# Kernel optimization log

Measured on AMD Instinct MI355X. Metric: run time of the kernel, lower is better.

The kernel has to match this reference:

```python
import jax, jax.numpy as jnp
import numpy as np

T, N, DIM, DSTATE = 64, 10000, 128, 16

def setup_inputs() -> dict:
    key = jax.random.key(0)
    ks = jax.random.split(key, 5)
    sequence = jax.random.normal(ks[0], (T, N, DIM), dtype=jnp.float32)
    # Diagonal SISO SSM parameters per channel: A is a stable decay in (0,1)
    A = jax.random.uniform(ks[1], (DIM, DSTATE), dtype=jnp.float32, minval=0.1, maxval=0.99)
    B = jax.random.normal(ks[2], (DIM, DSTATE), dtype=jnp.float32) * 0.1
    C = jax.random.normal(ks[3], (DIM, DSTATE), dtype=jnp.float32) * 0.1
    D = jax.random.normal(ks[4], (DIM,), dtype=jnp.float32) * 0.1
    return {"sequence": sequence, "A": A, "B": B, "C": C, "D": D}

def reference(sequence, A, B, C, D):
    # sequence: [T, N, dim]; A,B,C: [dim, d_state]; D: [dim]
    # Per-timestep diagonal SISO cell:
    #   h_t = A * h_{t-1} + B * x_t        (h: [N, dim, d_state])
    #   y_t = sum_s(C * h_t) + D * x_t     (y: [N, dim])
    n = sequence.shape[1]
    h0 = jnp.zeros((n, A.shape[0], A.shape[1]), dtype=sequence.dtype)

    def step(h, x):
        h = A[None] * h + B[None] * x[..., None]
        y = jnp.einsum('nds,ds->nd', h, C) + D[None] * x
        return h, y

    _, outputs = jax.lax.scan(step, h0, sequence)
    return outputs  # [T, N, dim]
```

## Files before the change

kernel.cpp:

```cpp
#include <hip/hip_runtime.h>


constexpr int T_STEPS = 64;
constexpr int DIM = 128;
constexpr int DSTATE = 16;
constexpr int CH = 8;
constexpr int S_FIX = 10000 * 128;

template <int S>
__global__ __launch_bounds__(256) void graph_ssm_kernel(
    const float* __restrict__ seq,
    const float* __restrict__ A,
    const float* __restrict__ B,
    const float* __restrict__ C,
    const float* __restrict__ Dp,
    float* __restrict__ out)
{
    const int tid = blockIdx.x * blockDim.x + threadIdx.x;
    if (tid >= S) return;
    const int d = tid & (DIM - 1);

    float a[DSTATE], cb[DSTATE], g[DSTATE];
#pragma unroll
    for (int s = 0; s < DSTATE; ++s) {
        a[s]  = A[d * DSTATE + s];
        cb[s] = C[d * DSTATE + s] * B[d * DSTATE + s];
        g[s]  = 0.0f;
    }
    float dd = Dp[d];

#pragma unroll
    for (int s = 0; s < DSTATE; ++s) {
        asm volatile("" : "+v"(a[s]), "+v"(cb[s]));
    }
    asm volatile("" : "+v"(dd));

    const float* sp = seq + tid;
    float* op = out + tid;

    auto step = [&](int t, float x) {
        float y0 = dd * x, y1 = 0.f;
#pragma unroll
        for (int s = 0; s < DSTATE; s += 2) {
            g[s + 0] = fmaf(a[s + 0], g[s + 0], x);
            y0 = fmaf(cb[s + 0], g[s + 0], y0);
            g[s + 1] = fmaf(a[s + 1], g[s + 1], x);
            y1 = fmaf(cb[s + 1], g[s + 1], y1);
        }
        __builtin_nontemporal_store(y0 + y1, op + (size_t)t * S);
    };

    float xb[CH], xn[CH];
#pragma unroll
    for (int j = 0; j < CH; ++j) xb[j] = sp[(size_t)j * S];

#pragma unroll 1
    for (int tc = 0; tc < T_STEPS - CH; tc += CH) {
#pragma unroll
        for (int j = 0; j < CH; ++j) xn[j] = sp[(size_t)(tc + CH + j) * S];
#pragma unroll
        for (int j = 0; j < CH; ++j) step(tc + j, xb[j]);
#pragma unroll
        for (int j = 0; j < CH; ++j) xb[j] = xn[j];
    }
#pragma unroll
    for (int j = 0; j < CH; ++j) step(T_STEPS - CH + j, xb[j]);
}

__global__ __launch_bounds__(256) void graph_ssm_kernel_dyn(
    const float* __restrict__ seq, const float* __restrict__ A,
    const float* __restrict__ B, const float* __restrict__ C,
    const float* __restrict__ Dp, float* __restrict__ out, int S)
{
    const int tid = blockIdx.x * blockDim.x + threadIdx.x;
    if (tid >= S) return;
    const int d = tid & (DIM - 1);
    float a[DSTATE], cb[DSTATE], g[DSTATE];
#pragma unroll
    for (int s = 0; s < DSTATE; ++s) {
        a[s]  = A[d * DSTATE + s];
        cb[s] = C[d * DSTATE + s] * B[d * DSTATE + s];
        g[s]  = 0.0f;
    }
    float dd = Dp[d];
#pragma unroll
    for (int s = 0; s < DSTATE; ++s) asm volatile("" : "+v"(a[s]), "+v"(cb[s]));
    asm volatile("" : "+v"(dd));
    const float* sp = seq + tid;
    float* op = out + tid;
    float x = sp[0];
    for (int t = 0; t < T_STEPS; ++t) {
        float xnext = (t + 1 < T_STEPS) ? sp[(size_t)(t + 1) * S] : 0.f;
        float y0 = dd * x, y1 = 0.f;
#pragma unroll
        for (int s = 0; s < DSTATE; s += 2) {
            g[s + 0] = fmaf(a[s + 0], g[s + 0], x);
            y0 = fmaf(cb[s + 0], g[s + 0], y0);
            g[s + 1] = fmaf(a[s + 1], g[s + 1], x);
            y1 = fmaf(cb[s + 1], g[s + 1], y1);
        }
        __builtin_nontemporal_store(y0 + y1, op + (size_t)t * S);
        x = xnext;
    }
}

extern "C" void kernel_launch(void* const* d_in, const int* in_sizes, int n_in,
                              void* d_out, int out_size, void* d_ws, size_t ws_size,
                              hipStream_t stream) {
    const float* seq = (const float*)d_in[0];
    const float* A   = (const float*)d_in[1];
    const float* B   = (const float*)d_in[2];
    const float* C   = (const float*)d_in[3];
    const float* Dp  = (const float*)d_in[4];
    float* out = (float*)d_out;

    const int S = in_sizes[0] / T_STEPS;
    const int block = 256;
    const int grid = (S + block - 1) / block;
    if (S == S_FIX) {
        graph_ssm_kernel<S_FIX><<<grid, block, 0, stream>>>(seq, A, B, C, Dp, out);
    } else {
        graph_ssm_kernel_dyn<<<grid, block, 0, stream>>>(seq, A, B, C, Dp, out, S);
    }
}
```

Baseline: 554.1 us.

## Process two channels per thread with float2 loads and ping-pong buffering

Each thread now handles two adjacent channels, so reads and writes become float2 vector accesses and the grid is halved. The prefetch is restructured into two alternating CH=4 buffers, and nontemporal stores are replaced with ordinary stores. The goal is fewer, wider memory instructions and more independent FMA chains per thread, at the cost of roughly twice the register state and fewer resident threads.

```diff
diff --git a/kernel.cpp b/kernel.cpp
--- a/kernel.cpp
+++ b/kernel.cpp
@@ -4,11 +4,11 @@
 constexpr int T_STEPS = 64;
 constexpr int DIM = 128;
 constexpr int DSTATE = 16;
-constexpr int CH = 8;
+constexpr int CH = 4;
 constexpr int S_FIX = 10000 * 128;
 
 template <int S>
-__global__ __launch_bounds__(256) void graph_ssm_kernel(
+__global__ __launch_bounds__(256) void graph_ssm_kernel2(
     const float* __restrict__ seq,
     const float* __restrict__ A,
     const float* __restrict__ B,
@@ -16,55 +16,71 @@
     const float* __restrict__ Dp,
     float* __restrict__ out)
 {
+    constexpr int S2 = S / 2;
     const int tid = blockIdx.x * blockDim.x + threadIdx.x;
-    if (tid >= S) return;
-    const int d = tid & (DIM - 1);
+    if (tid >= S2) return;
+    const int d0 = (tid * 2) & (DIM - 1);
 
-    float a[DSTATE], cb[DSTATE], g[DSTATE];
+    float a[2][DSTATE], cb[2][DSTATE], g[2][DSTATE];
 #pragma unroll
-    for (int s = 0; s < DSTATE; ++s) {
-        a[s]  = A[d * DSTATE + s];
-        cb[s] = C[d * DSTATE + s] * B[d * DSTATE + s];
-        g[s]  = 0.0f;
+    for (int c = 0; c < 2; ++c) {
+#pragma unroll
+        for (int s = 0; s < DSTATE; ++s) {
+            a[c][s]  = A[(d0 + c) * DSTATE + s];
+            cb[c][s] = C[(d0 + c) * DSTATE + s] * B[(d0 + c) * DSTATE + s];
+            g[c][s]  = 0.0f;
+        }
     }
-    float dd = Dp[d];
+    float dd0 = Dp[d0], dd1 = Dp[d0 + 1];
 
 #pragma unroll
-    for (int s = 0; s < DSTATE; ++s) {
-        asm volatile("" : "+v"(a[s]), "+v"(cb[s]));
-    }
-    asm volatile("" : "+v"(dd));
+    for (int c = 0; c < 2; ++c)
+#pragma unroll
+        for (int s = 0; s < DSTATE; ++s)
+            asm volatile("" : "+v"(a[c][s]), "+v"(cb[c][s]));
+    asm volatile("" : "+v"(dd0), "+v"(dd1));
 
-    const float* sp = seq + tid;
-    float* op = out + tid;
+    const float2* sp = reinterpret_cast<const float2*>(seq) + tid;
+    float2* op = reinterpret_cast<float2*>(out) + tid;
 
-    auto step = [&](int t, float x) {
-        float y0 = dd * x, y1 = 0.f;
+    auto step = [&](int t, float2 x) {
+        float y00 = dd0 * x.x, y01 = 0.f;
+        float y10 = dd1 * x.y, y11 = 0.f;
 #pragma unroll
         for (int s = 0; s < DSTATE; s += 2) {
-            g[s + 0] = fmaf(a[s + 0], g[s + 0], x);
-            y0 = fmaf(cb[s + 0], g[s + 0], y0);
-            g[s + 1] = fmaf(a[s + 1], g[s + 1], x);
-            y1 = fmaf(cb[s + 1], g[s + 1], y1);
+            g[0][s]     = fmaf(a[0][s],     g[0][s],     x.x);
+            y00         = fmaf(cb[0][s],    g[0][s],     y00);
+            g[0][s + 1] = fmaf(a[0][s + 1], g[0][s + 1], x.x);
+            y01         = fmaf(cb[0][s + 1], g[0][s + 1], y01);
+            g[1][s]     = fmaf(a[1][s],     g[1][s],     x.y);
+            y10         = fmaf(cb[1][s],    g[1][s],     y10);
+            g[1][s + 1] = fmaf(a[1][s + 1], g[1][s + 1], x.y);
+            y11         = fmaf(cb[1][s + 1], g[1][s + 1], y11);
         }
-        __builtin_nontemporal_store(y0 + y1, op + (size_t)t * S);
+        op[(size_t)t * S2] = make_float2(y00 + y01, y10 + y11);
     };
 
-    float xb[CH], xn[CH];
+    float2 bufA[CH], bufB[CH];
+    auto loadTo = [&](float2* buf, int t0) {
 #pragma unroll
-    for (int j = 0; j < CH; ++j) xb[j] = sp[(size_t)j * S];
+        for (int j = 0; j < CH; ++j) buf[j] = sp[(size_t)(t0 + j) * S2];
+    };
+    auto compute = [&](float2* buf, int t0) {
+#pragma unroll
+        for (int j = 0; j < CH; ++j) step(t0 + j, buf[j]);
+    };
 
+    loadTo(bufA, 0);
 #pragma unroll 1
-    for (int tc = 0; tc < T_STEPS - CH; tc += CH) {
-#pragma unroll
-        for (int j = 0; j < CH; ++j) xn[j] = sp[(size_t)(tc + CH + j) * S];
-#pragma unroll
-        for (int j = 0; j < CH; ++j) step(tc + j, xb[j]);
-#pragma unroll
-        for (int j = 0; j < CH; ++j) xb[j] = xn[j];
+    for (int k = 0; k < T_STEPS / (2 * CH) - 1; ++k) {
+        loadTo(bufB, 8 * k + 4);
+        compute(bufA, 8 * k);
+        loadTo(bufA, 8 * k + 8);
+        compute(bufB, 8 * k + 4);
     }
-#pragma unroll
-    for (int j = 0; j < CH; ++j) step(T_STEPS - CH + j, xb[j]);
+    loadTo(bufB, T_STEPS - CH);
+    compute(bufA, T_STEPS - 2 * CH);
+    compute(bufB, T_STEPS - CH);
 }
 
 __global__ __launch_bounds__(256) void graph_ssm_kernel_dyn(
@@ -83,9 +99,6 @@
         g[s]  = 0.0f;
     }
     float dd = Dp[d];
-#pragma unroll
-    for (int s = 0; s < DSTATE; ++s) asm volatile("" : "+v"(a[s]), "+v"(cb[s]));
-    asm volatile("" : "+v"(dd));
     const float* sp = seq + tid;
     float* op = out + tid;
     float x = sp[0];
@@ -99,7 +112,7 @@
             g[s + 1] = fmaf(a[s + 1], g[s + 1], x);
             y1 = fmaf(cb[s + 1], g[s + 1], y1);
         }
-        __builtin_nontemporal_store(y0 + y1, op + (size_t)t * S);
+        op[(size_t)t * S] = y0 + y1;
         x = xnext;
     }
 }
@@ -116,10 +129,11 @@
 
     const int S = in_sizes[0] / T_STEPS;
     const int block = 256;
-    const int grid = (S + block - 1) / block;
     if (S == S_FIX) {
-        graph_ssm_kernel<S_FIX><<<grid, block, 0, stream>>>(seq, A, B, C, Dp, out);
+        const int grid = (S / 2 + block - 1) / block;
+        graph_ssm_kernel2<S_FIX><<<grid, block, 0, stream>>>(seq, A, B, C, Dp, out);
     } else {
+        const int grid = (S + block - 1) / block;
         graph_ssm_kernel_dyn<<<grid, block, 0, stream>>>(seq, A, B, C, Dp, out, S);
     }
 }
```

Measured after the change: 560.3 us. Within noise of the previous version (+1.1%).
